# Kernel optimization log

Measured on AMD Instinct MI355X. Metric: run time of the kernel, lower is better.

Reference implementation:

```python
import jax, jax.numpy as jnp
import numpy as np

GRID_SIZE = 5
SPLINE_ORDER = 3
NUM_COEFF = GRID_SIZE + SPLINE_ORDER  # 8
L = 3
B, I, H = 4096, 256, 512
EPS = 1e-5


def make_grid(in_features):
    # efficient-kan default grid over [-1, 1] extended by spline_order knots each side
    h = 2.0 / GRID_SIZE
    g = jnp.arange(-SPLINE_ORDER, GRID_SIZE + SPLINE_ORDER + 1, dtype=jnp.float32) * h - 1.0
    return jnp.broadcast_to(g, (in_features, g.shape[0]))  # (in, G+2k+1)


def b_splines(x, grid):
    # x: (B, in), grid: (in, G+2k+1) -> (B, in, G+k) via Cox-de-Boor recursion
    xg = x[..., None]
    bases = ((xg >= grid[:, :-1]) & (xg < grid[:, 1:])).astype(x.dtype)
    for j in range(1, SPLINE_ORDER + 1):
        left = (xg - grid[:, :-(j + 1)]) / (grid[:, j:-1] - grid[:, :-(j + 1)])
        right = (grid[:, j + 1:] - xg) / (grid[:, j + 1:] - grid[:, 1:-j])
        bases = left * bases[..., :-1] + right * bases[..., 1:]
    return bases


def kan_linear(x, base_w, spline_w, grid):
    # base path: SiLU(x) @ W_base^T ; spline path: sum over (in, coeff)
    base = jax.nn.silu(x) @ base_w.T
    spl = jnp.einsum('bik,oik->bo', b_splines(x, grid), spline_w)
    return base + spl


def layer_norm(x, g, b):
    mu = jnp.mean(x, axis=-1, keepdims=True)
    var = jnp.var(x, axis=-1, keepdims=True)
    return (x - mu) / jnp.sqrt(var + EPS) * g + b


def _sublayer(z_prev, wx_b, wx_s, wh_b, wh_s, hz_b, hz_s, phi_b, phi_s,
              hh_w, hh_b, ln_g, ln_b, x_t, grid_in, grid_h):
    s_t = kan_linear(x_t, wx_b, wx_s, grid_in) + kan_linear(z_prev, wh_b, wh_s, grid_h)
    o_t = kan_linear(s_t, phi_b, phi_s, grid_h)
    z_t = layer_norm(z_prev @ hh_w.T + hh_b + kan_linear(o_t, hz_b, hz_s, grid_h), ln_g, ln_b)
    return o_t, z_t


def setup_inputs() -> dict:
    key = jax.random.key(0)
    ks = jax.random.split(key, 24)
    s = 0.05  # small init to keep gates/splines in sane range
    inp = {
        'x_t': jax.random.normal(ks[0], (B, I), jnp.float32),
        'h_prev': jax.random.normal(ks[1], (B, H), jnp.float32),
        'c_prev': jax.random.normal(ks[2], (B, H), jnp.float32),
        'z_prev': jax.random.normal(ks[3], (L, B, H), jnp.float32),
        'wx_base': jax.random.normal(ks[4], (L, H, I), jnp.float32) * s,
        'wx_spline': jax.random.normal(ks[5], (L, H, I, NUM_COEFF), jnp.float32) * s,
        'wh_base': jax.random.normal(ks[6], (L, H, H), jnp.float32) * s,
        'wh_spline': jax.random.normal(ks[7], (L, H, H, NUM_COEFF), jnp.float32) * s,
        'hz_base': jax.random.normal(ks[8], (L, H, H), jnp.float32) * s,
        'hz_spline': jax.random.normal(ks[9], (L, H, H, NUM_COEFF), jnp.float32) * s,
        'phi_base': jax.random.normal(ks[10], (L, H, H), jnp.float32) * s,
        'phi_spline': jax.random.normal(ks[11], (L, H, H, NUM_COEFF), jnp.float32) * s,
        'hh_w': jax.random.normal(ks[12], (L, H, H), jnp.float32) * s,
        'hh_b': jax.random.normal(ks[13], (L, H), jnp.float32) * s,
        'ln_g': jnp.ones((L, H), jnp.float32),
        'ln_b': jnp.zeros((L, H), jnp.float32),
        'f_w': jax.random.normal(ks[14], (H, I + H), jnp.float32) * s,
        'f_b': jax.random.normal(ks[15], (H,), jnp.float32) * s,
        'i_w': jax.random.normal(ks[16], (H, I + H), jnp.float32) * s,
        'i_b': jax.random.normal(ks[17], (H,), jnp.float32) * s,
        'g_w': jax.random.normal(ks[18], (H, I + H), jnp.float32) * s,
        'g_b': jax.random.normal(ks[19], (H,), jnp.float32) * s,
        'o_w': jax.random.normal(ks[20], (H, L * H), jnp.float32) * s,
        'o_b': jax.random.normal(ks[21], (H,), jnp.float32) * s,
    }
    return inp


def reference(x_t, h_prev, c_prev, z_prev, wx_base, wx_spline, wh_base, wh_spline,
              hz_base, hz_spline, phi_base, phi_spline, hh_w, hh_b, ln_g, ln_b,
              f_w, f_b, i_w, i_b, g_w, g_b, o_w, o_b):
    grid_in = make_grid(I)
    grid_h = make_grid(H)
    cat = jnp.concatenate([x_t, h_prev], axis=-1)  # (B, I+H)
    f_t = jax.nn.sigmoid(cat @ f_w.T + f_b)
    i_t = jax.nn.sigmoid(cat @ i_w.T + i_b)
    g_t = jnp.tanh(cat @ g_w.T + g_b)
    # vmap the RKAN sublayer over the L stacked sublayers
    sub = jax.vmap(_sublayer, in_axes=(0,) * 13 + (None, None, None))
    o_all, z_all = sub(z_prev, wx_base, wx_spline, wh_base, wh_spline,
                       hz_base, hz_spline, phi_base, phi_spline,
                       hh_w, hh_b, ln_g, ln_b, x_t, grid_in, grid_h)
    # concat sublayer phi outputs: (L,B,H) -> (B, L*H)
    r_t = jnp.transpose(o_all, (1, 0, 2)).reshape(B, L * H)
    o_t = jax.nn.sigmoid(r_t @ o_w.T + o_b)
    c_t = f_t * c_prev + i_t * g_t
    h_t = o_t * jnp.tanh(c_t)
    return h_t, c_t, z_all
```

## Files before the change

### kernel.cpp

```cpp
#include <hip/hip_runtime.h>

typedef __attribute__((ext_vector_type(8))) short short8;
typedef __attribute__((ext_vector_type(4))) short short4v;
typedef __attribute__((ext_vector_type(4))) float floatx4;

__device__ inline short f2bf(float v) {
    unsigned u = __builtin_bit_cast(unsigned, v);
    unsigned r = (u + 0x7fffu + ((u >> 16) & 1u)) >> 16;
    return (short)r;
}
__device__ inline float bf2f(short s) {
    unsigned u = ((unsigned)(unsigned short)s) << 16;
    return __builtin_bit_cast(float, u);
}
__device__ inline short4v pack4(float4 v) {
    short4v o;
    o[0] = f2bf(v.x); o[1] = f2bf(v.y); o[2] = f2bf(v.z); o[3] = f2bf(v.w);
    return o;
}
__device__ inline short4v silu4(float4 v) {
    float4 s;
    s.x = v.x / (1.f + __expf(-v.x));
    s.y = v.y / (1.f + __expf(-v.y));
    s.z = v.z / (1.f + __expf(-v.z));
    s.w = v.w / (1.f + __expf(-v.w));
    return pack4(s);
}

__device__ inline void spline8(float v, short* arr) {
    float u = (v + 2.2f) * 2.5f;
    float fj = floorf(u);
    int jj = (int)fj;
    float t1 = u - fj;
    float ok = (jj >= 0 && jj <= 10) ? (1.f / 6.f) : 0.f;
    float t2 = t1 * t1, t3 = t2 * t1;
    float omt = 1.f - t1;
    short sw0 = f2bf(omt * omt * omt * ok);
    short sw1 = f2bf((3.f * t3 - 6.f * t2 + 4.f) * ok);
    short sw2 = f2bf((-3.f * t3 + 3.f * t2 + 3.f * t1 + 1.f) * ok);
    short sw3 = f2bf(t3 * ok);
#pragma unroll
    for (int s = 0; s < 8; ++s) {
        int rr = s - jj + 3;
        arr[s] = (rr == 0) ? sw0 : (rr == 1) ? sw1 : (rr == 2) ? sw2
                 : (rr == 3) ? sw3 : (short)0;
    }
}
__device__ inline void expand4(float4 v, short* silu_dst, short* spl_dst) {
    *(short4v*)silu_dst = silu4(v);
    short arr[8];
    spline8(v.x, arr); *(short8*)(spl_dst)      = *(const short8*)arr;
    spline8(v.y, arr); *(short8*)(spl_dst + 8)  = *(const short8*)arr;
    spline8(v.z, arr); *(short8*)(spl_dst + 16) = *(const short8*)arr;
    spline8(v.w, arr); *(short8*)(spl_dst + 24) = *(const short8*)arr;
}

__global__ __launch_bounds__(256, 3) void gemm128(
    int S, int Kh,
    const short* __restrict__ A0, int lda0, long sA0, int K0,
    const short* __restrict__ W0, int ldw0, long sW0,
    const short* __restrict__ A1, int lda1, long sA1, int K1,
    const short* __restrict__ W1, int ldw1, long sW1,
    float* __restrict__ C, int ldc, long sC, long sSplit)
{
    __shared__ short As[128 * 64];
    __shared__ short Ws[128 * 64];
    const int t = threadIdx.x;
    int n = blockIdx.x + (blockIdx.y << 5) + (blockIdx.z << 7);
    int k8 = n & 7, j = n >> 3;
    int byi = j & 3;
    int t2 = j >> 2;
    int bxi = k8 * 4 + (t2 & 3);
    int bzi = t2 >> 2;
    const int z = bzi / S, s = bzi % S;
    const int bm = bxi * 128, bn = byi * 128;
    const int lane = t & 63, w = t >> 6;
    const int wm = (w >> 1) * 64, wn = (w & 1) * 64;
    const int lrow = lane & 15, quad = lane >> 4;

    floatx4 acc[4][4] = {};

    const int kbeg = s * Kh, kend = kbeg + Kh;

    const short* A = A0 + (long)z * sA0;
    const short* W = W0 + (long)z * sW0;
    int lda = lda0, ldw = ldw0;
    int kb = kbeg, ke = (kend < K0) ? kend : K0;

    for (int seg = 0; seg < 2; ++seg) {
        for (int kv = kb; kv < ke; kv += 64) {
#pragma unroll
            for (int i = 0; i < 4; ++i) {
                int c = i * 256 + t;
                int row = c >> 3;
                int cg = ((c ^ row) & 7) * 8;
                const short* gp = A + (long)(bm + row) * lda + kv + cg;
                __builtin_amdgcn_global_load_lds(
                    (const __attribute__((address_space(1))) void*)gp,
                    (__attribute__((address_space(3))) void*)(As + c * 8), 16, 0, 0);
                const short* gq = W + (long)(bn + row) * ldw + kv + cg;
                __builtin_amdgcn_global_load_lds(
                    (const __attribute__((address_space(1))) void*)gq,
                    (__attribute__((address_space(3))) void*)(Ws + c * 8), 16, 0, 0);
            }
            __syncthreads();
#pragma unroll
            for (int kk = 0; kk < 2; ++kk) {
                short8 af[4], bfr[4];
#pragma unroll
                for (int mi = 0; mi < 4; ++mi) {
                    int r = wm + mi * 16 + lrow;
                    af[mi] = *(const short8*)(As + r * 64 +
                                              (((kk * 4 + quad) ^ (r & 7)) * 8));
                }
#pragma unroll
                for (int ni = 0; ni < 4; ++ni) {
                    int r = wn + ni * 16 + lrow;
                    bfr[ni] = *(const short8*)(Ws + r * 64 +
                                               (((kk * 4 + quad) ^ (r & 7)) * 8));
                }
#pragma unroll
                for (int mi = 0; mi < 4; ++mi)
#pragma unroll
                    for (int ni = 0; ni < 4; ++ni)
                        acc[mi][ni] = __builtin_amdgcn_mfma_f32_16x16x32_bf16(
                            af[mi], bfr[ni], acc[mi][ni], 0, 0, 0);
            }
            __syncthreads();
        }
        A = A1 + (long)z * sA1;
        W = W1 + (long)z * sW1;
        lda = lda1; ldw = ldw1;
        kb = ((kbeg > K0) ? kbeg : K0) - K0;
        ke = kend - K0;
    }

    float* Cz = C + (long)z * sC + (long)s * sSplit;
#pragma unroll
    for (int mi = 0; mi < 4; ++mi)
#pragma unroll
        for (int ni = 0; ni < 4; ++ni)
#pragma unroll
            for (int r = 0; r < 4; ++r) {
                int row = bm + wm + mi * 16 + quad * 4 + r;
                int col = bn + wn + ni * 16 + lrow;
                Cz[(long)row * ldc + col] = acc[mi][ni][r];
            }
}

__global__ __launch_bounds__(256) void gemm64(
    const short* __restrict__ A0, int lda0, long sA0, int K0,
    const short* __restrict__ W0, int ldw0, long sW0,
    short* __restrict__ C, int ldc, long sC)
{
    __shared__ short As[64 * 64];
    __shared__ short Ws[128 * 64];
    const int t = threadIdx.x;
    const int z = blockIdx.z;
    const int bm = blockIdx.x * 64;
    const int bn = blockIdx.y * 128;
    const int lane = t & 63, w = t >> 6;
    const int wm = (w >> 1) * 32, wn = (w & 1) * 64;
    const int lrow = lane & 15, quad = lane >> 4;

    floatx4 acc[2][4] = {};

    const short* A = A0 + (long)z * sA0;
    const short* W = W0 + (long)z * sW0;

    for (int k0 = 0; k0 < K0; k0 += 64) {
#pragma unroll
        for (int i = 0; i < 2; ++i) {
            int c = i * 256 + t;
            int row = c >> 3;
            int cg = ((c ^ row) & 7) * 8;
            const short* gp = A + (long)(bm + row) * lda0 + k0 + cg;
            __builtin_amdgcn_global_load_lds(
                (const __attribute__((address_space(1))) void*)gp,
                (__attribute__((address_space(3))) void*)(As + c * 8), 16, 0, 0);
        }
#pragma unroll
        for (int i = 0; i < 4; ++i) {
            int c = i * 256 + t;
            int row = c >> 3;
            int cg = ((c ^ row) & 7) * 8;
            const short* gq = W + (long)(bn + row) * ldw0 + k0 + cg;
            __builtin_amdgcn_global_load_lds(
                (const __attribute__((address_space(1))) void*)gq,
                (__attribute__((address_space(3))) void*)(Ws + c * 8), 16, 0, 0);
        }
        __syncthreads();
#pragma unroll
        for (int kk = 0; kk < 2; ++kk) {
            short8 af[2], bfr[4];
#pragma unroll
            for (int mi = 0; mi < 2; ++mi) {
                int r = wm + mi * 16 + lrow;
                af[mi] = *(const short8*)(As + r * 64 +
                                          (((kk * 4 + quad) ^ (r & 7)) * 8));
            }
#pragma unroll
            for (int ni = 0; ni < 4; ++ni) {
                int r = wn + ni * 16 + lrow;
                bfr[ni] = *(const short8*)(Ws + r * 64 +
                                           (((kk * 4 + quad) ^ (r & 7)) * 8));
            }
#pragma unroll
            for (int mi = 0; mi < 2; ++mi)
#pragma unroll
                for (int ni = 0; ni < 4; ++ni)
                    acc[mi][ni] = __builtin_amdgcn_mfma_f32_16x16x32_bf16(
                        af[mi], bfr[ni], acc[mi][ni], 0, 0, 0);
        }
        __syncthreads();
    }

    short* Cz = C + (long)z * sC;
#pragma unroll
    for (int mi = 0; mi < 2; ++mi)
#pragma unroll
        for (int ni = 0; ni < 4; ++ni)
#pragma unroll
            for (int r = 0; r < 4; ++r) {
                int row = bm + wm + mi * 16 + quad * 4 + r;
                int col = bn + wn + ni * 16 + lrow;
                Cz[(long)row * ldc + col] = f2bf(acc[mi][ni][r]);
            }
}

__global__ __launch_bounds__(256) void megapack8(
    const float* __restrict__ wx_b, const float* __restrict__ wx_s,
    const float* __restrict__ wh_b, const float* __restrict__ wh_s,
    const float* __restrict__ hz_b, const float* __restrict__ hz_s,
    const float* __restrict__ phi_b, const float* __restrict__ phi_s,
    const float* __restrict__ hh_w, const float* __restrict__ o_w,
    const float* __restrict__ f_w, const float* __restrict__ i_w,
    const float* __restrict__ g_w,
    short* __restrict__ Wx, short* __restrict__ Wh, short* __restrict__ Whz,
    short* __restrict__ Wphi, short* __restrict__ HHb, short* __restrict__ OWb,
    short* __restrict__ Wg)
{
    int bid = blockIdx.x, tid = threadIdx.x;
    const float* sp;
    short* dst;
    long e;
    if (bid < 1728) {
        e = ((long)bid * 256 + tid) * 8;
        int r = (int)(e / 2304), c = (int)(e % 2304);
        sp = (c < 256) ? wx_b + (long)r * 256 + c
                       : wx_s + (long)r * 2048 + (c - 256);
        dst = Wx + e;
    } else if (bid < 12096) {
        int jb = bid - 1728;
        int job = jb / 3456, lb = jb % 3456;
        const float* bp = (job == 0) ? wh_b : (job == 1) ? hz_b : phi_b;
        const float* spw = (job == 0) ? wh_s : (job == 1) ? hz_s : phi_s;
        short* dp = (job == 0) ? Wh : (job == 1) ? Whz : Wphi;
        e = ((long)lb * 256 + tid) * 8;
        int r = (int)(e / 4608), c = (int)(e % 4608);
        sp = (c < 512) ? bp + (long)r * 512 + c
                       : spw + (long)r * 4096 + (c - 512);
        dst = dp + e;
    } else if (bid < 12480) {
        e = ((long)(bid - 12096) * 256 + tid) * 8;
        sp = hh_w + e; dst = HHb + e;
    } else if (bid < 12864) {
        e = ((long)(bid - 12480) * 256 + tid) * 8;
        sp = o_w + e; dst = OWb + e;
    } else if (bid < 13056) {
        e = ((long)(bid - 12864) * 256 + tid) * 8;
        sp = f_w + e; dst = Wg + e;
    } else if (bid < 13248) {
        e = ((long)(bid - 13056) * 256 + tid) * 8;
        sp = i_w + e; dst = Wg + 393216 + e;
    } else {
        e = ((long)(bid - 13248) * 256 + tid) * 8;
        sp = g_w + e; dst = Wg + 786432 + e;
    }
    float4 a = *(const float4*)sp;
    float4 b = *(const float4*)(sp + 4);
    short8 o;
    o[0] = f2bf(a.x); o[1] = f2bf(a.y); o[2] = f2bf(a.z); o[3] = f2bf(a.w);
    o[4] = f2bf(b.x); o[5] = f2bf(b.y); o[6] = f2bf(b.z); o[7] = f2bf(b.w);
    *(short8*)dst = o;
}

__global__ __launch_bounds__(256) void prep_acts4(
    const float* __restrict__ x_t, const float* __restrict__ h_prev,
    const float* __restrict__ z_prev,
    short* __restrict__ Xe, short* __restrict__ Agate,
    short* __restrict__ Ze, short* __restrict__ zraw)
{
    int bid = blockIdx.x, tid = threadIdx.x;
    if (bid < 1024) {
        int r = (bid << 2) + (tid >> 6);
        int i = (tid & 63) << 2;
        float4 v = *(const float4*)(x_t + (long)r * 256 + i);
        *(short4v*)(Agate + (long)r * 768 + i) = pack4(v);
        long ob = (long)r * 2304;
        expand4(v, Xe + ob + i, Xe + ob + 256 + (long)i * 8);
    } else if (bid < 3072) {
        long idx = ((long)(bid - 1024) * 256 + tid) * 4;
        float4 v = *(const float4*)(h_prev + idx);
        long b = idx >> 9; int hh = (int)(idx & 511);
        *(short4v*)(Agate + b * 768 + 256 + hh) = pack4(v);
    } else {
        int j = bid - 3072;
        int r = (j << 1) + (tid >> 7);
        int i = (tid & 127) << 2;
        float4 v = *(const float4*)(z_prev + (long)r * 512 + i);
        *(short4v*)(zraw + (long)r * 512 + i) = pack4(v);
        long ob = (long)r * 4608;
        expand4(v, Ze + ob + i, Ze + ob + 512 + (long)i * 8);
    }
}

__global__ __launch_bounds__(256) void expand_pair4(
    const float* __restrict__ P, long sSplit, int S,
    short* __restrict__ out, short* __restrict__ compact)
{
    int tid = threadIdx.x;
    int r = (blockIdx.x << 1) + (tid >> 7);
    int i = (tid & 127) << 2;
    long idx = (long)r * 512 + i;
    float4 v = *(const float4*)(P + idx);
    for (int s = 1; s < S; ++s) {
        float4 a = *(const float4*)(P + idx + (long)s * sSplit);
        v.x += a.x; v.y += a.y; v.z += a.z; v.w += a.w;
    }
    if (compact) *(short4v*)(compact + idx) = pack4(v);
    long ob = (long)r * 4608;
    expand4(v, out + ob + i, out + ob + 512 + (long)i * 8);
}

__global__ __launch_bounds__(256) void ln_wave(const float* __restrict__ P,
                                               long sSplit, int S,
                                               const float* __restrict__ hh_b,
                                               const float* __restrict__ ln_g,
                                               const float* __restrict__ ln_b,
                                               float* __restrict__ out)
{
    int wv = threadIdx.x >> 6, lane = threadIdx.x & 63;
    int row = blockIdx.x * 4 + wv;
    int l = row >> 12;
    int col = lane * 8;
    long base = (long)row * 512 + col;
    float v[8];
#pragma unroll
    for (int e = 0; e < 8; ++e) v[e] = hh_b[l * 512 + col + e];
    for (int s = 0; s < S; ++s) {
        float4 a = *(const float4*)(P + base + (long)s * sSplit);
        float4 b = *(const float4*)(P + base + 4 + (long)s * sSplit);
        v[0] += a.x; v[1] += a.y; v[2] += a.z; v[3] += a.w;
        v[4] += b.x; v[5] += b.y; v[6] += b.z; v[7] += b.w;
    }
    float sm = 0.f, sq = 0.f;
#pragma unroll
    for (int e = 0; e < 8; ++e) { sm += v[e]; sq += v[e] * v[e]; }
#pragma unroll
    for (int off = 32; off; off >>= 1) {
        sm += __shfl_down(sm, off);
        sq += __shfl_down(sq, off);
    }
    sm = __shfl(sm, 0);
    sq = __shfl(sq, 0);
    float mu = sm * (1.f / 512.f);
    float var = sq * (1.f / 512.f) - mu * mu;
    float rstd = rsqrtf(var + 1e-5f);
    float o[8];
#pragma unroll
    for (int e = 0; e < 8; ++e)
        o[e] = (v[e] - mu) * rstd * ln_g[l * 512 + col + e] + ln_b[l * 512 + col + e];
    float* op = out + base;
    *(float4*)op = make_float4(o[0], o[1], o[2], o[3]);
    *(float4*)(op + 4) = make_float4(o[4], o[5], o[6], o[7]);
}

__global__ __launch_bounds__(256) void cell_epilogue(const short* __restrict__ gates,
                                                     const short* __restrict__ opre,
                                                     const float* __restrict__ c_prev,
                                                     const float* __restrict__ f_b,
                                                     const float* __restrict__ i_b,
                                                     const float* __restrict__ g_b,
                                                     const float* __restrict__ o_b,
                                                     float* __restrict__ out)
{
    long idx = blockIdx.x * 256L + threadIdx.x;
    long b = idx >> 9; int h = (int)(idx & 511);
    const short* g = gates + b * 1536;
    float fp = bf2f(g[h]) + f_b[h];
    float ip = bf2f(g[512 + h]) + i_b[h];
    float gp = bf2f(g[1024 + h]) + g_b[h];
    float op = bf2f(opre[idx]) + o_b[h];
    float ft = 1.f / (1.f + __expf(-fp));
    float it = 1.f / (1.f + __expf(-ip));
    float gt = tanhf(gp);
    float ot = 1.f / (1.f + __expf(-op));
    float c = ft * c_prev[idx] + it * gt;
    out[idx] = ot * tanhf(c);
    out[idx + 2097152] = c;
}

extern "C" void kernel_launch(void* const* d_in, const int* in_sizes, int n_in,
                              void* d_out, int out_size, void* d_ws, size_t ws_size,
                              hipStream_t stream)
{
    const float* x_t       = (const float*)d_in[0];
    const float* h_prev    = (const float*)d_in[1];
    const float* c_prev    = (const float*)d_in[2];
    const float* z_prev    = (const float*)d_in[3];
    const float* wx_base   = (const float*)d_in[4];
    const float* wx_spline = (const float*)d_in[5];
    const float* wh_base   = (const float*)d_in[6];
    const float* wh_spline = (const float*)d_in[7];
    const float* hz_base   = (const float*)d_in[8];
    const float* hz_spline = (const float*)d_in[9];
    const float* phi_base  = (const float*)d_in[10];
    const float* phi_spline= (const float*)d_in[11];
    const float* hh_w      = (const float*)d_in[12];
    const float* hh_b      = (const float*)d_in[13];
    const float* ln_g      = (const float*)d_in[14];
    const float* ln_b      = (const float*)d_in[15];
    const float* f_w       = (const float*)d_in[16];
    const float* f_b       = (const float*)d_in[17];
    const float* i_w       = (const float*)d_in[18];
    const float* i_b       = (const float*)d_in[19];
    const float* g_w       = (const float*)d_in[20];
    const float* g_b       = (const float*)d_in[21];
    const float* o_w       = (const float*)d_in[22];
    const float* o_b       = (const float*)d_in[23];
    float* out = (float*)d_out;
    const long BH = 4096L * 512;

    char* p = (char*)d_ws;
    auto alloc = [&](size_t bytes) {
        char* q = p;
        p += (bytes + 255) & ~(size_t)255;
        return q;
    };

    short* Wx   = (short*)alloc(3L * 512 * 2304 * 2);
    short* Wh   = (short*)alloc(3L * 512 * 4608 * 2);
    short* Whz  = (short*)alloc(3L * 512 * 4608 * 2);
    short* Wphi = (short*)alloc(3L * 512 * 4608 * 2);
    short* HHb  = (short*)alloc(3L * 512 * 512 * 2);
    short* OWb  = (short*)alloc(512L * 1536 * 2);
    short* Wg   = (short*)alloc(1536L * 768 * 2);
    short* Agate= (short*)alloc(4096L * 768 * 2);
    short* zraw = (short*)alloc(3L * 4096 * 512 * 2);
    short* XR   = (short*)alloc(4096L * 2304 * 2);
    short* Ebuf = (short*)alloc(3L * 4096 * 4608 * 2);

    const int S = 2;
    const long PS = 3L * 4096 * 512;
    float* Pbuf = (float*)alloc((size_t)S * PS * 4);

    short* Xe = XR;
    short* Rbuf = XR;
    short* gbuf = Ebuf;
    short* opre = Ebuf + 4096L * 1536;

    megapack8<<<13440, 256, 0, stream>>>(
        wx_base, wx_spline, wh_base, wh_spline, hz_base, hz_spline,
        phi_base, phi_spline, hh_w, o_w, f_w, i_w, g_w,
        Wx, Wh, Whz, Wphi, HHb, OWb, Wg);

    prep_acts4<<<9216, 256, 0, stream>>>(x_t, h_prev, z_prev, Xe, Agate, Ebuf, zraw);

    gemm128<<<dim3(32, 4, 3 * S), 256, 0, stream>>>(S, 3456,
        Xe, 2304, 0, 2304,                 Wx, 2304, 512L * 2304,
        Ebuf, 4608, 4096L * 4608, 4608,    Wh, 4608, 512L * 4608,
        Pbuf, 512, 4096L * 512, PS);

    expand_pair4<<<6144, 256, 0, stream>>>(Pbuf, PS, S, Ebuf, (short*)0);

    gemm128<<<dim3(32, 4, 3 * S), 256, 0, stream>>>(S, 2304,
        Ebuf, 4608, 4096L * 4608, 4608,    Wphi, 4608, 512L * 4608,
        zraw, 0, 0, 0,                     Wphi, 0, 0,
        Pbuf, 1536, 512, PS);

    expand_pair4<<<6144, 256, 0, stream>>>(Pbuf, PS, S, Ebuf, Rbuf);

    gemm128<<<dim3(32, 4, 3 * S), 256, 0, stream>>>(S, 2560,
        Ebuf, 13824, 4608, 4608,           Whz, 4608, 512L * 4608,
        zraw, 512, 4096L * 512, 512,       HHb, 512, 512L * 512,
        Pbuf, 512, 4096L * 512, PS);

    ln_wave<<<3072, 256, 0, stream>>>(Pbuf, PS, S, hh_b, ln_g, ln_b, out + 2 * BH);

    gemm64<<<dim3(64, 12, 1), 256, 0, stream>>>(
        Agate, 768, 0, 768,  Wg, 768, 0,
        gbuf, 1536, 0);

    gemm64<<<dim3(64, 4, 1), 256, 0, stream>>>(
        Rbuf, 1536, 0, 1536, OWb, 1536, 0,
        opre, 512, 0);

    cell_epilogue<<<8192, 256, 0, stream>>>(gbuf, opre, c_prev, f_b, i_b, g_b, o_b, out);
}
```

Measured before the change: 705.3 us.

## Fuse whole pipeline into one cooperative persistent kernel with grid syncs

Replaces the chain of separate kernel launches with a single cooperative kernel of 768 blocks that runs weight packing, activation prep, the three KAN GEMMs, spline expansion, the gate GEMMs, layernorm and the cell epilogue, separated by grid-wide barriers. The gate GEMMs now use the 128-tile GEMM with bf16 output instead of the separate 64-row GEMM, and the cell epilogue is vectorised by four. The aim is to remove per-launch overhead and tail gaps between stages. In exchange, grid syncs add barrier cost, the persistent loops cap parallelism at 768 blocks for the elementwise phases, and a non-cooperative fallback path is kept.

```diff
diff --git a/kernel.cpp b/kernel.cpp
--- a/kernel.cpp
+++ b/kernel.cpp
@@ -1,8 +1,13 @@
 #include <hip/hip_runtime.h>
+#include <hip/hip_cooperative_groups.h>
+
+namespace cg = cooperative_groups;
 
 typedef __attribute__((ext_vector_type(8))) short short8;
 typedef __attribute__((ext_vector_type(4))) short short4v;
 typedef __attribute__((ext_vector_type(4))) float floatx4;
+
+static constexpr long PS = 3L * 4096 * 512;
 
 __device__ inline short f2bf(float v) {
     unsigned u = __builtin_bit_cast(unsigned, v);
@@ -55,23 +60,31 @@
     spline8(v.w, arr); *(short8*)(spl_dst + 24) = *(const short8*)arr;
 }
 
-__global__ __launch_bounds__(256, 3) void gemm128(
-    int S, int Kh,
+struct MP {
+    const float *x_t, *h_prev, *c_prev, *z_prev;
+    const float *wx_b, *wx_s, *wh_b, *wh_s, *hz_b, *hz_s, *phi_b, *phi_s;
+    const float *hh_w, *hh_b, *ln_g, *ln_b;
+    const float *f_w, *f_b, *i_w, *i_b, *g_w, *g_b, *o_w, *o_b;
+    float* out;
+    short *Wx, *Wh, *Whz, *Wphi, *HHb, *OWb, *Wg, *Agate, *zraw, *XR, *Ebuf;
+    float* Pbuf;
+};
+
+__device__ void gemm_tile(short* As, short* Ws, int t, int n,
+    int nbx, int nby, int S, int Kh,
     const short* __restrict__ A0, int lda0, long sA0, int K0,
     const short* __restrict__ W0, int ldw0, long sW0,
-    const short* __restrict__ A1, int lda1, long sA1, int K1,
+    const short* __restrict__ A1, int lda1, long sA1,
     const short* __restrict__ W1, int ldw1, long sW1,
-    float* __restrict__ C, int ldc, long sC, long sSplit)
-{
-    __shared__ short As[128 * 64];
-    __shared__ short Ws[128 * 64];
-    const int t = threadIdx.x;
-    int n = blockIdx.x + (blockIdx.y << 5) + (blockIdx.z << 7);
+    float* __restrict__ C, short* __restrict__ Cb,
+    int ldc, long sC, long sSplit)
+{
     int k8 = n & 7, j = n >> 3;
-    int byi = j & 3;
-    int t2 = j >> 2;
-    int bxi = k8 * 4 + (t2 & 3);
-    int bzi = t2 >> 2;
+    int byi = j % nby;
+    int j2 = j / nby;
+    int mper = nbx >> 3;
+    int bxi = k8 * mper + (j2 % mper);
+    int bzi = j2 / mper;
     const int z = bzi / S, s = bzi % S;
     const int bm = bxi * 128, bn = byi * 128;
     const int lane = t & 63, w = t >> 6;
@@ -135,127 +148,49 @@
         ke = kend - K0;
     }
 
-    float* Cz = C + (long)z * sC + (long)s * sSplit;
-#pragma unroll
-    for (int mi = 0; mi < 4; ++mi)
-#pragma unroll
-        for (int ni = 0; ni < 4; ++ni)
-#pragma unroll
-            for (int r = 0; r < 4; ++r) {
-                int row = bm + wm + mi * 16 + quad * 4 + r;
-                int col = bn + wn + ni * 16 + lrow;
-                Cz[(long)row * ldc + col] = acc[mi][ni][r];
-            }
-}
-
-__global__ __launch_bounds__(256) void gemm64(
-    const short* __restrict__ A0, int lda0, long sA0, int K0,
-    const short* __restrict__ W0, int ldw0, long sW0,
-    short* __restrict__ C, int ldc, long sC)
-{
-    __shared__ short As[64 * 64];
-    __shared__ short Ws[128 * 64];
-    const int t = threadIdx.x;
-    const int z = blockIdx.z;
-    const int bm = blockIdx.x * 64;
-    const int bn = blockIdx.y * 128;
-    const int lane = t & 63, w = t >> 6;
-    const int wm = (w >> 1) * 32, wn = (w & 1) * 64;
-    const int lrow = lane & 15, quad = lane >> 4;
-
-    floatx4 acc[2][4] = {};
-
-    const short* A = A0 + (long)z * sA0;
-    const short* W = W0 + (long)z * sW0;
-
-    for (int k0 = 0; k0 < K0; k0 += 64) {
-#pragma unroll
-        for (int i = 0; i < 2; ++i) {
-            int c = i * 256 + t;
-            int row = c >> 3;
-            int cg = ((c ^ row) & 7) * 8;
-            const short* gp = A + (long)(bm + row) * lda0 + k0 + cg;
-            __builtin_amdgcn_global_load_lds(
-                (const __attribute__((address_space(1))) void*)gp,
-                (__attribute__((address_space(3))) void*)(As + c * 8), 16, 0, 0);
-        }
-#pragma unroll
-        for (int i = 0; i < 4; ++i) {
-            int c = i * 256 + t;
-            int row = c >> 3;
-            int cg = ((c ^ row) & 7) * 8;
-            const short* gq = W + (long)(bn + row) * ldw0 + k0 + cg;
-            __builtin_amdgcn_global_load_lds(
-                (const __attribute__((address_space(1))) void*)gq,
-                (__attribute__((address_space(3))) void*)(Ws + c * 8), 16, 0, 0);
-        }
-        __syncthreads();
-#pragma unroll
-        for (int kk = 0; kk < 2; ++kk) {
-            short8 af[2], bfr[4];
-#pragma unroll
-            for (int mi = 0; mi < 2; ++mi) {
-                int r = wm + mi * 16 + lrow;
-                af[mi] = *(const short8*)(As + r * 64 +
-                                          (((kk * 4 + quad) ^ (r & 7)) * 8));
-            }
-#pragma unroll
-            for (int ni = 0; ni < 4; ++ni) {
-                int r = wn + ni * 16 + lrow;
-                bfr[ni] = *(const short8*)(Ws + r * 64 +
-                                           (((kk * 4 + quad) ^ (r & 7)) * 8));
-            }
-#pragma unroll
-            for (int mi = 0; mi < 2; ++mi)
-#pragma unroll
-                for (int ni = 0; ni < 4; ++ni)
-                    acc[mi][ni] = __builtin_amdgcn_mfma_f32_16x16x32_bf16(
-                        af[mi], bfr[ni], acc[mi][ni], 0, 0, 0);
-        }
-        __syncthreads();
-    }
-
-    short* Cz = C + (long)z * sC;
-#pragma unroll
-    for (int mi = 0; mi < 2; ++mi)
-#pragma unroll
-        for (int ni = 0; ni < 4; ++ni)
-#pragma unroll
-            for (int r = 0; r < 4; ++r) {
-                int row = bm + wm + mi * 16 + quad * 4 + r;
-                int col = bn + wn + ni * 16 + lrow;
-                Cz[(long)row * ldc + col] = f2bf(acc[mi][ni][r]);
-            }
-}
-
-__global__ __launch_bounds__(256) void megapack8(
-    const float* __restrict__ wx_b, const float* __restrict__ wx_s,
-    const float* __restrict__ wh_b, const float* __restrict__ wh_s,
-    const float* __restrict__ hz_b, const float* __restrict__ hz_s,
-    const float* __restrict__ phi_b, const float* __restrict__ phi_s,
-    const float* __restrict__ hh_w, const float* __restrict__ o_w,
-    const float* __restrict__ f_w, const float* __restrict__ i_w,
-    const float* __restrict__ g_w,
-    short* __restrict__ Wx, short* __restrict__ Wh, short* __restrict__ Whz,
-    short* __restrict__ Wphi, short* __restrict__ HHb, short* __restrict__ OWb,
-    short* __restrict__ Wg)
-{
-    int bid = blockIdx.x, tid = threadIdx.x;
+    if (C) {
+        float* Cz = C + (long)z * sC + (long)s * sSplit;
+#pragma unroll
+        for (int mi = 0; mi < 4; ++mi)
+#pragma unroll
+            for (int ni = 0; ni < 4; ++ni)
+#pragma unroll
+                for (int r = 0; r < 4; ++r) {
+                    int row = bm + wm + mi * 16 + quad * 4 + r;
+                    int col = bn + wn + ni * 16 + lrow;
+                    Cz[(long)row * ldc + col] = acc[mi][ni][r];
+                }
+    } else {
+        short* Cz = Cb + (long)z * sC;
+#pragma unroll
+        for (int mi = 0; mi < 4; ++mi)
+#pragma unroll
+            for (int ni = 0; ni < 4; ++ni)
+#pragma unroll
+                for (int r = 0; r < 4; ++r) {
+                    int row = bm + wm + mi * 16 + quad * 4 + r;
+                    int col = bn + wn + ni * 16 + lrow;
+                    Cz[(long)row * ldc + col] = f2bf(acc[mi][ni][r]);
+                }
+    }
+}
+
+__device__ __forceinline__ void megapack_body(int bid, int tid, const MP& p) {
     const float* sp;
     short* dst;
     long e;
     if (bid < 1728) {
         e = ((long)bid * 256 + tid) * 8;
         int r = (int)(e / 2304), c = (int)(e % 2304);
-        sp = (c < 256) ? wx_b + (long)r * 256 + c
-                       : wx_s + (long)r * 2048 + (c - 256);
-        dst = Wx + e;
+        sp = (c < 256) ? p.wx_b + (long)r * 256 + c
+                       : p.wx_s + (long)r * 2048 + (c - 256);
+        dst = p.Wx + e;
     } else if (bid < 12096) {
         int jb = bid - 1728;
         int job = jb / 3456, lb = jb % 3456;
-        const float* bp = (job == 0) ? wh_b : (job == 1) ? hz_b : phi_b;
-        const float* spw = (job == 0) ? wh_s : (job == 1) ? hz_s : phi_s;
-        short* dp = (job == 0) ? Wh : (job == 1) ? Whz : Wphi;
+        const float* bp = (job == 0) ? p.wh_b : (job == 1) ? p.hz_b : p.phi_b;
+        const float* spw = (job == 0) ? p.wh_s : (job == 1) ? p.hz_s : p.phi_s;
+        short* dp = (job == 0) ? p.Wh : (job == 1) ? p.Whz : p.Wphi;
         e = ((long)lb * 256 + tid) * 8;
         int r = (int)(e / 4608), c = (int)(e % 4608);
         sp = (c < 512) ? bp + (long)r * 512 + c
@@ -263,19 +198,19 @@
         dst = dp + e;
     } else if (bid < 12480) {
         e = ((long)(bid - 12096) * 256 + tid) * 8;
-        sp = hh_w + e; dst = HHb + e;
+        sp = p.hh_w + e; dst = p.HHb + e;
     } else if (bid < 12864) {
         e = ((long)(bid - 12480) * 256 + tid) * 8;
-        sp = o_w + e; dst = OWb + e;
+        sp = p.o_w + e; dst = p.OWb + e;
     } else if (bid < 13056) {
         e = ((long)(bid - 12864) * 256 + tid) * 8;
-        sp = f_w + e; dst = Wg + e;
+        sp = p.f_w + e; dst = p.Wg + e;
     } else if (bid < 13248) {
         e = ((long)(bid - 13056) * 256 + tid) * 8;
-        sp = i_w + e; dst = Wg + 393216 + e;
+        sp = p.i_w + e; dst = p.Wg + 393216 + e;
     } else {
         e = ((long)(bid - 13248) * 256 + tid) * 8;
-        sp = g_w + e; dst = Wg + 786432 + e;
+        sp = p.g_w + e; dst = p.Wg + 786432 + e;
     }
     float4 a = *(const float4*)sp;
     float4 b = *(const float4*)(sp + 4);
@@ -285,42 +220,35 @@
     *(short8*)dst = o;
 }
 
-__global__ __launch_bounds__(256) void prep_acts4(
-    const float* __restrict__ x_t, const float* __restrict__ h_prev,
-    const float* __restrict__ z_prev,
-    short* __restrict__ Xe, short* __restrict__ Agate,
-    short* __restrict__ Ze, short* __restrict__ zraw)
-{
-    int bid = blockIdx.x, tid = threadIdx.x;
+__device__ __forceinline__ void prep_body(int bid, int tid, const MP& p) {
     if (bid < 1024) {
         int r = (bid << 2) + (tid >> 6);
         int i = (tid & 63) << 2;
-        float4 v = *(const float4*)(x_t + (long)r * 256 + i);
-        *(short4v*)(Agate + (long)r * 768 + i) = pack4(v);
+        float4 v = *(const float4*)(p.x_t + (long)r * 256 + i);
+        *(short4v*)(p.Agate + (long)r * 768 + i) = pack4(v);
         long ob = (long)r * 2304;
-        expand4(v, Xe + ob + i, Xe + ob + 256 + (long)i * 8);
+        expand4(v, p.XR + ob + i, p.XR + ob + 256 + (long)i * 8);
     } else if (bid < 3072) {
         long idx = ((long)(bid - 1024) * 256 + tid) * 4;
-        float4 v = *(const float4*)(h_prev + idx);
+        float4 v = *(const float4*)(p.h_prev + idx);
         long b = idx >> 9; int hh = (int)(idx & 511);
-        *(short4v*)(Agate + b * 768 + 256 + hh) = pack4(v);
+        *(short4v*)(p.Agate + b * 768 + 256 + hh) = pack4(v);
     } else {
-        int j = bid - 3072;
-        int r = (j << 1) + (tid >> 7);
+        int jz = bid - 3072;
+        int r = (jz << 1) + (tid >> 7);
         int i = (tid & 127) << 2;
-        float4 v = *(const float4*)(z_prev + (long)r * 512 + i);
-        *(short4v*)(zraw + (long)r * 512 + i) = pack4(v);
+        float4 v = *(const float4*)(p.z_prev + (long)r * 512 + i);
+        *(short4v*)(p.zraw + (long)r * 512 + i) = pack4(v);
         long ob = (long)r * 4608;
-        expand4(v, Ze + ob + i, Ze + ob + 512 + (long)i * 8);
-    }
-}
-
-__global__ __launch_bounds__(256) void expand_pair4(
+        expand4(v, p.Ebuf + ob + i, p.Ebuf + ob + 512 + (long)i * 8);
+    }
+}
+
+__device__ __forceinline__ void expand_body(int vb, int tid,
     const float* __restrict__ P, long sSplit, int S,
     short* __restrict__ out, short* __restrict__ compact)
 {
-    int tid = threadIdx.x;
-    int r = (blockIdx.x << 1) + (tid >> 7);
+    int r = (vb << 1) + (tid >> 7);
     int i = (tid & 127) << 2;
     long idx = (long)r * 512 + i;
     float4 v = *(const float4*)(P + idx);
@@ -333,15 +261,13 @@
     expand4(v, out + ob + i, out + ob + 512 + (long)i * 8);
 }
 
-__global__ __launch_bounds__(256) void ln_wave(const float* __restrict__ P,
-                                               long sSplit, int S,
-                                               const float* __restrict__ hh_b,
-                                               const float* __restrict__ ln_g,
-                                               const float* __restrict__ ln_b,
-                                               float* __restrict__ out)
-{
-    int wv = threadIdx.x >> 6, lane = threadIdx.x & 63;
-    int row = blockIdx.x * 4 + wv;
+__device__ __forceinline__ void ln_body(int vb, int tid,
+    const float* __restrict__ P, long sSplit, int S,
+    const float* __restrict__ hh_b, const float* __restrict__ ln_g,
+    const float* __restrict__ ln_b, float* __restrict__ out)
+{
+    int wv = tid >> 6, lane = tid & 63;
+    int row = vb * 4 + wv;
     int l = row >> 12;
     int col = lane * 8;
     long base = (long)row * 512 + col;
@@ -376,125 +302,208 @@
     *(float4*)(op + 4) = make_float4(o[4], o[5], o[6], o[7]);
 }
 
-__global__ __launch_bounds__(256) void cell_epilogue(const short* __restrict__ gates,
-                                                     const short* __restrict__ opre,
-                                                     const float* __restrict__ c_prev,
-                                                     const float* __restrict__ f_b,
-                                                     const float* __restrict__ i_b,
-                                                     const float* __restrict__ g_b,
-                                                     const float* __restrict__ o_b,
-                                                     float* __restrict__ out)
-{
-    long idx = blockIdx.x * 256L + threadIdx.x;
-    long b = idx >> 9; int h = (int)(idx & 511);
-    const short* g = gates + b * 1536;
-    float fp = bf2f(g[h]) + f_b[h];
-    float ip = bf2f(g[512 + h]) + i_b[h];
-    float gp = bf2f(g[1024 + h]) + g_b[h];
-    float op = bf2f(opre[idx]) + o_b[h];
-    float ft = 1.f / (1.f + __expf(-fp));
-    float it = 1.f / (1.f + __expf(-ip));
-    float gt = tanhf(gp);
-    float ot = 1.f / (1.f + __expf(-op));
-    float c = ft * c_prev[idx] + it * gt;
-    out[idx] = ot * tanhf(c);
-    out[idx + 2097152] = c;
+__device__ __forceinline__ void cell_body(int vb, int tid, const MP& p) {
+    long e = ((long)vb * 256 + tid) * 4;
+    long b = e >> 9; int h = (int)(e & 511);
+    const short* g = p.Ebuf + b * 1536;
+    short4v gf = *(const short4v*)(g + h);
+    short4v gi = *(const short4v*)(g + 512 + h);
+    short4v gg = *(const short4v*)(g + 1024 + h);
+    short4v go = *(const short4v*)(p.Ebuf + 4096L * 1536 + e);
+    float4 cp = *(const float4*)(p.c_prev + e);
+    float cpv[4] = { cp.x, cp.y, cp.z, cp.w };
+    float hv[4], cv[4];
+#pragma unroll
+    for (int q = 0; q < 4; ++q) {
+        float fp = bf2f(gf[q]) + p.f_b[h + q];
+        float ip = bf2f(gi[q]) + p.i_b[h + q];
+        float gp = bf2f(gg[q]) + p.g_b[h + q];
+        float op = bf2f(go[q]) + p.o_b[h + q];
+        float ft = 1.f / (1.f + __expf(-fp));
+        float it = 1.f / (1.f + __expf(-ip));
+        float gt = tanhf(gp);
+        float ot = 1.f / (1.f + __expf(-op));
+        float c = ft * cpv[q] + it * gt;
+        cv[q] = c;
+        hv[q] = ot * tanhf(c);
+    }
+    *(float4*)(p.out + e) = make_float4(hv[0], hv[1], hv[2], hv[3]);
+    *(float4*)(p.out + e + 2097152) = make_float4(cv[0], cv[1], cv[2], cv[3]);
+}
+
+__global__ __launch_bounds__(256, 3) void mega(MP p)
+{
+    __shared__ short As[128 * 64];
+    __shared__ short Ws[128 * 64];
+    cg::grid_group grid = cg::this_grid();
+    const int bid = blockIdx.x, tid = threadIdx.x;
+
+    for (int vb = bid; vb < 22656; vb += 768) {
+        if (vb < 13440) megapack_body(vb, tid, p);
+        else            prep_body(vb - 13440, tid, p);
+    }
+    __threadfence(); grid.sync(); __threadfence();
+
+    gemm_tile(As, Ws, tid, bid, 32, 4, 2, 3456,
+              p.XR, 2304, 0, 2304,            p.Wx, 2304, 512L * 2304,
+              p.Ebuf, 4608, 4096L * 4608,     p.Wh, 4608, 512L * 4608,
+              p.Pbuf, (short*)0, 512, 4096L * 512, PS);
+    __threadfence(); grid.sync(); __threadfence();
+
+    for (int vb = bid; vb < 6144; vb += 768)
+        expand_body(vb, tid, p.Pbuf, PS, 2, p.Ebuf, (short*)0);
+    __threadfence(); grid.sync(); __threadfence();
+
+    gemm_tile(As, Ws, tid, bid, 32, 4, 2, 2304,
+              p.Ebuf, 4608, 4096L * 4608, 4608,   p.Wphi, 4608, 512L * 4608,
+              p.Ebuf, 4608, 4096L * 4608,         p.Wphi, 4608, 512L * 4608,
+              p.Pbuf, (short*)0, 1536, 512, PS);
+    __threadfence(); grid.sync(); __threadfence();
+
+    for (int vb = bid; vb < 6144; vb += 768)
+        expand_body(vb, tid, p.Pbuf, PS, 2, p.Ebuf, p.XR);
+    __threadfence(); grid.sync(); __threadfence();
+
+    gemm_tile(As, Ws, tid, bid, 32, 4, 2, 2560,
+              p.Ebuf, 13824, 4608, 4608,      p.Whz, 4608, 512L * 4608,
+              p.zraw, 512, 4096L * 512,       p.HHb, 512, 512L * 512,
+              p.Pbuf, (short*)0, 512, 4096L * 512, PS);
+    __threadfence(); grid.sync(); __threadfence();
+
+    if (bid < 384)
+        gemm_tile(As, Ws, tid, bid, 32, 12, 1, 768,
+                  p.Agate, 768, 0, 768,   p.Wg, 768, 0,
+                  p.Agate, 768, 0,        p.Wg, 768, 0,
+                  (float*)0, p.Ebuf, 1536, 0, 0);
+    else if (bid < 512)
+        gemm_tile(As, Ws, tid, bid - 384, 32, 4, 1, 1536,
+                  p.XR, 1536, 0, 1536,    p.OWb, 1536, 0,
+                  p.XR, 1536, 0,          p.OWb, 1536, 0,
+                  (float*)0, p.Ebuf + 4096L * 1536, 512, 0, 0);
+    __threadfence(); grid.sync(); __threadfence();
+
+    for (int vb = bid; vb < 5120; vb += 768) {
+        if (vb < 3072) ln_body(vb, tid, p.Pbuf, PS, 2,
+                               p.hh_b, p.ln_g, p.ln_b, p.out + 4194304L);
+        else           cell_body(vb - 3072, tid, p);
+    }
+}
+
+__global__ __launch_bounds__(256) void kprep(MP p) {
+    int vb = blockIdx.x;
+    if (vb < 13440) megapack_body(vb, threadIdx.x, p);
+    else            prep_body(vb - 13440, threadIdx.x, p);
+}
+
+__global__ __launch_bounds__(256, 3) void kgemm(
+    int nbx, int nby, int S, int Kh,
+    const short* __restrict__ A0, int lda0, long sA0, int K0,
+    const short* __restrict__ W0, int ldw0, long sW0,
+    const short* __restrict__ A1, int lda1, long sA1,
+    const short* __restrict__ W1, int ldw1, long sW1,
+    float* __restrict__ C, short* __restrict__ Cb, int ldc, long sC, long sSplit)
+{
+    __shared__ short As[128 * 64];
+    __shared__ short Ws[128 * 64];
+    gemm_tile(As, Ws, threadIdx.x, blockIdx.x, nbx, nby, S, Kh,
+              A0, lda0, sA0, K0, W0, ldw0, sW0,
+              A1, lda1, sA1, W1, ldw1, sW1, C, Cb, ldc, sC, sSplit);
+}
+
+__global__ __launch_bounds__(256) void kexpand(
+    const float* __restrict__ P, long sSplit, int S,
+    short* __restrict__ out, short* __restrict__ compact)
+{
+    expand_body(blockIdx.x, threadIdx.x, P, sSplit, S, out, compact);
+}
+
+__global__ __launch_bounds__(256) void kfin(MP p) {
+    int vb = blockIdx.x;
+    if (vb < 3072) ln_body(vb, threadIdx.x, p.Pbuf, PS, 2,
+                           p.hh_b, p.ln_g, p.ln_b, p.out + 4194304L);
+    else           cell_body(vb - 3072, threadIdx.x, p);
 }
 
 extern "C" void kernel_launch(void* const* d_in, const int* in_sizes, int n_in,
                               void* d_out, int out_size, void* d_ws, size_t ws_size,
                               hipStream_t stream)
 {
-    const float* x_t       = (const float*)d_in[0];
-    const float* h_prev    = (const float*)d_in[1];
-    const float* c_prev    = (const float*)d_in[2];
-    const float* z_prev    = (const float*)d_in[3];
-    const float* wx_base   = (const float*)d_in[4];
-    const float* wx_spline = (const float*)d_in[5];
-    const float* wh_base   = (const float*)d_in[6];
-    const float* wh_spline = (const float*)d_in[7];
-    const float* hz_base   = (const float*)d_in[8];
-    const float* hz_spline = (const float*)d_in[9];
-    const float* phi_base  = (const float*)d_in[10];
-    const float* phi_spline= (const float*)d_in[11];
-    const float* hh_w      = (const float*)d_in[12];
-    const float* hh_b      = (const float*)d_in[13];
-    const float* ln_g      = (const float*)d_in[14];
-    const float* ln_b      = (const float*)d_in[15];
-    const float* f_w       = (const float*)d_in[16];
-    const float* f_b       = (const float*)d_in[17];
-    const float* i_w       = (const float*)d_in[18];
-    const float* i_b       = (const float*)d_in[19];
-    const float* g_w       = (const float*)d_in[20];
-    const float* g_b       = (const float*)d_in[21];
-    const float* o_w       = (const float*)d_in[22];
-    const float* o_b       = (const float*)d_in[23];
-    float* out = (float*)d_out;
-    const long BH = 4096L * 512;
-
-    char* p = (char*)d_ws;
+    char* wp = (char*)d_ws;
     auto alloc = [&](size_t bytes) {
-        char* q = p;
-        p += (bytes + 255) & ~(size_t)255;
+        char* q = wp;
+        wp += (bytes + 255) & ~(size_t)255;
         return q;
     };
 
-    short* Wx   = (short*)alloc(3L * 512 * 2304 * 2);
-    short* Wh   = (short*)alloc(3L * 512 * 4608 * 2);
-    short* Whz  = (short*)alloc(3L * 512 * 4608 * 2);
-    short* Wphi = (short*)alloc(3L * 512 * 4608 * 2);
-    short* HHb  = (short*)alloc(3L * 512 * 512 * 2);
-    short* OWb  = (short*)alloc(512L * 1536 * 2);
-    short* Wg   = (short*)alloc(1536L * 768 * 2);
-    short* Agate= (short*)alloc(4096L * 768 * 2);
-    short* zraw = (short*)alloc(3L * 4096 * 512 * 2);
-    short* XR   = (short*)alloc(4096L * 2304 * 2);
-    short* Ebuf = (short*)alloc(3L * 4096 * 4608 * 2);
-
-    const int S = 2;
-    const long PS = 3L * 4096 * 512;
-    float* Pbuf = (float*)alloc((size_t)S * PS * 4);
-
-    short* Xe = XR;
-    short* Rbuf = XR;
-    short* gbuf = Ebuf;
-    short* opre = Ebuf + 4096L * 1536;
-
-    megapack8<<<13440, 256, 0, stream>>>(
-        wx_base, wx_spline, wh_base, wh_spline, hz_base, hz_spline,
-        phi_base, phi_spline, hh_w, o_w, f_w, i_w, g_w,
-        Wx, Wh, Whz, Wphi, HHb, OWb, Wg);
-
-    prep_acts4<<<9216, 256, 0, stream>>>(x_t, h_prev, z_prev, Xe, Agate, Ebuf, zraw);
-
-    gemm128<<<dim3(32, 4, 3 * S), 256, 0, stream>>>(S, 3456,
-        Xe, 2304, 0, 2304,                 Wx, 2304, 512L * 2304,
-        Ebuf, 4608, 4096L * 4608, 4608,    Wh, 4608, 512L * 4608,
-        Pbuf, 512, 4096L * 512, PS);
-
-    expand_pair4<<<6144, 256, 0, stream>>>(Pbuf, PS, S, Ebuf, (short*)0);
-
-    gemm128<<<dim3(32, 4, 3 * S), 256, 0, stream>>>(S, 2304,
-        Ebuf, 4608, 4096L * 4608, 4608,    Wphi, 4608, 512L * 4608,
-        zraw, 0, 0, 0,                     Wphi, 0, 0,
-        Pbuf, 1536, 512, PS);
-
-    expand_pair4<<<6144, 256, 0, stream>>>(Pbuf, PS, S, Ebuf, Rbuf);
-
-    gemm128<<<dim3(32, 4, 3 * S), 256, 0, stream>>>(S, 2560,
-        Ebuf, 13824, 4608, 4608,           Whz, 4608, 512L * 4608,
-        zraw, 512, 4096L * 512, 512,       HHb, 512, 512L * 512,
-        Pbuf, 512, 4096L * 512, PS);
-
-    ln_wave<<<3072, 256, 0, stream>>>(Pbuf, PS, S, hh_b, ln_g, ln_b, out + 2 * BH);
-
-    gemm64<<<dim3(64, 12, 1), 256, 0, stream>>>(
-        Agate, 768, 0, 768,  Wg, 768, 0,
-        gbuf, 1536, 0);
-
-    gemm64<<<dim3(64, 4, 1), 256, 0, stream>>>(
-        Rbuf, 1536, 0, 1536, OWb, 1536, 0,
-        opre, 512, 0);
-
-    cell_epilogue<<<8192, 256, 0, stream>>>(gbuf, opre, c_prev, f_b, i_b, g_b, o_b, out);
-}
+    MP p;
+    p.x_t    = (const float*)d_in[0];
+    p.h_prev = (const float*)d_in[1];
+    p.c_prev = (const float*)d_in[2];
+    p.z_prev = (const float*)d_in[3];
+    p.wx_b   = (const float*)d_in[4];
+    p.wx_s   = (const float*)d_in[5];
+    p.wh_b   = (const float*)d_in[6];
+    p.wh_s   = (const float*)d_in[7];
+    p.hz_b   = (const float*)d_in[8];
+    p.hz_s   = (const float*)d_in[9];
+    p.phi_b  = (const float*)d_in[10];
+    p.phi_s  = (const float*)d_in[11];
+    p.hh_w   = (const float*)d_in[12];
+    p.hh_b   = (const float*)d_in[13];
+    p.ln_g   = (const float*)d_in[14];
+    p.ln_b   = (const float*)d_in[15];
+    p.f_w    = (const float*)d_in[16];
+    p.f_b    = (const float*)d_in[17];
+    p.i_w    = (const float*)d_in[18];
+    p.i_b    = (const float*)d_in[19];
+    p.g_w    = (const float*)d_in[20];
+    p.g_b    = (const float*)d_in[21];
+    p.o_w    = (const float*)d_in[22];
+    p.o_b    = (const float*)d_in[23];
+    p.out    = (float*)d_out;
+
+    p.Wx    = (short*)alloc(3L * 512 * 2304 * 2);
+    p.Wh    = (short*)alloc(3L * 512 * 4608 * 2);
+    p.Whz   = (short*)alloc(3L * 512 * 4608 * 2);
+    p.Wphi  = (short*)alloc(3L * 512 * 4608 * 2);
+    p.HHb   = (short*)alloc(3L * 512 * 512 * 2);
+    p.OWb   = (short*)alloc(512L * 1536 * 2);
+    p.Wg    = (short*)alloc(1536L * 768 * 2);
+    p.Agate = (short*)alloc(4096L * 768 * 2);
+    p.zraw  = (short*)alloc(3L * 4096 * 512 * 2);
+    p.XR    = (short*)alloc(4096L * 2304 * 2);
+    p.Ebuf  = (short*)alloc(3L * 4096 * 4608 * 2);
+    p.Pbuf  = (float*)alloc(2L * PS * 4);
+
+    void* kargs[] = { (void*)&p };
+    hipError_t err = hipLaunchCooperativeKernel(
+        (const void*)mega, dim3(768), dim3(256), kargs, 0, stream);
+
+    if (err != hipSuccess) {
+        (void)hipGetLastError();
+        kprep<<<22656, 256, 0, stream>>>(p);
+        kgemm<<<768, 256, 0, stream>>>(32, 4, 2, 3456,
+            p.XR, 2304, 0L, 2304,           p.Wx, 2304, 512L * 2304,
+            p.Ebuf, 4608, 4096L * 4608,     p.Wh, 4608, 512L * 4608,
+            p.Pbuf, (short*)0, 512, 4096L * 512, PS);
+        kexpand<<<6144, 256, 0, stream>>>(p.Pbuf, PS, 2, p.Ebuf, (short*)0);
+        kgemm<<<768, 256, 0, stream>>>(32, 4, 2, 2304,
+            p.Ebuf, 4608, 4096L * 4608, 4608,  p.Wphi, 4608, 512L * 4608,
+            p.Ebuf, 4608, 4096L * 4608,        p.Wphi, 4608, 512L * 4608,
+            p.Pbuf, (short*)0, 1536, 512, PS);
+        kexpand<<<6144, 256, 0, stream>>>(p.Pbuf, PS, 2, p.Ebuf, p.XR);
+        kgemm<<<768, 256, 0, stream>>>(32, 4, 2, 2560,
+            p.Ebuf, 13824, 4608, 4608,      p.Whz, 4608, 512L * 4608,
+            p.zraw, 512, 4096L * 512,       p.HHb, 512, 512L * 512,
+            p.Pbuf, (short*)0, 512, 4096L * 512, PS);
+        kgemm<<<384, 256, 0, stream>>>(32, 12, 1, 768,
+            p.Agate, 768, 0L, 768,          p.Wg, 768, 0L,
+            p.Agate, 768, 0L,               p.Wg, 768, 0L,
+            (float*)0, p.Ebuf, 1536, 0, 0);
+        kgemm<<<128, 256, 0, stream>>>(32, 4, 1, 1536,
+            p.XR, 1536, 0L, 1536,           p.OWb, 1536, 0L,
+            p.XR, 1536, 0L,                 p.OWb, 1536, 0L,
+            (float*)0, p.Ebuf + 4096L * 1536, 512, 0, 0);
+        kfin<<<5120, 256, 0, stream>>>(p);
+    }
+}
```

New measurement: 2.482 ms. 252% more time.
